# Performance work log

Measured on AMD Instinct MI355X. Metric: run time of the kernel, lower is better.

## Reference

```python
import jax, jax.numpy as jnp
import numpy as np

N, E = 50000, 800000
IN_FEATS, H, F = 128, 2, 64
NEG_SLOPE = 0.2


def _gat_conv(x, W, attn_l, attn_r, bias, src, dst):
    """DGL-style GATConv. x:[N,IN], W:[H*F,IN], attn_l/attn_r:[H,F], bias:[H*F]. Returns [N,H,F]."""
    z = (x @ W.T).reshape(N, H, F)                      # node projections
    el = jnp.einsum('nhf,hf->nh', z, attn_l)            # [N,H]
    er = jnp.einsum('nhf,hf->nh', z, attn_r)            # [N,H]
    e = jax.nn.leaky_relu(el[src] + er[dst], NEG_SLOPE) # [E,H] edge logits
    # edge softmax over incoming edges of each destination node
    m = jax.ops.segment_max(e, dst, num_segments=N)     # [N,H]
    ex = jnp.exp(e - m[dst])
    s = jax.ops.segment_sum(ex, dst, num_segments=N)    # [N,H]
    alpha = ex / s[dst]                                 # [E,H]
    msg = alpha[:, :, None] * z[src]                    # [E,H,F]
    out = jax.ops.segment_sum(msg, dst, num_segments=N) # [N,H,F]
    return out + bias.reshape(1, H, F)


def setup_inputs() -> dict:
    key = jax.random.key(0)
    ks = jax.random.split(key, 10)
    x = jax.random.normal(ks[0], (N, IN_FEATS), dtype=jnp.float32)
    h = jax.random.normal(ks[1], (N, H, F), dtype=jnp.float32)
    src = jax.random.randint(ks[2], (E,), 0, N, dtype=jnp.int32)
    dst = jax.random.randint(ks[3], (E,), 0, N, dtype=jnp.int32)
    sc = 1.0 / np.sqrt(IN_FEATS)
    W = jax.random.normal(ks[4], (3, H * F, IN_FEATS), dtype=jnp.float32) * sc  # r,u,c fc weights
    attn_l = jax.random.normal(ks[5], (3, H, F), dtype=jnp.float32) * 0.1
    attn_r = jax.random.normal(ks[6], (3, H, F), dtype=jnp.float32) * 0.1
    conv_bias = jax.random.normal(ks[7], (3, H * F), dtype=jnp.float32) * 0.02
    gate_bias = jax.random.uniform(ks[8], (3, H, F), dtype=jnp.float32)  # torch.rand init
    return {"x": x, "h": h, "W": W, "attn_l": attn_l, "attn_r": attn_r,
            "conv_bias": conv_bias, "gate_bias": gate_bias, "src": src, "dst": dst}


def reference(x, h, W, attn_l, attn_r, conv_bias, gate_bias, src, dst):
    # r, u, c gates; each GATConv is applied to x (use_hidden=False branch)
    r = jax.nn.sigmoid(_gat_conv(x, W[0], attn_l[0], attn_r[0], conv_bias[0], src, dst) + gate_bias[0])
    u = jax.nn.sigmoid(_gat_conv(x, W[1], attn_l[1], attn_r[1], conv_bias[1], src, dst) + gate_bias[1])
    # note: original computes h_ = r*h but never uses it in this branch (dead code)
    c = jax.nn.sigmoid(_gat_conv(x, W[2], attn_l[2], attn_r[2], conv_bias[2], src, dst) + gate_bias[2])
    new_h = u * h + (1.0 - u) * c
    return new_h
```

## Files before the change

### kernel.cpp

```cpp
#include <hip/hip_runtime.h>
#include <hip/hip_bf16.h>
#include <math.h>

#define NN 50000
#define EE 800000
#define KIN 128
#define HFD 128
#define ZB 256
#define NB 196
#define GB2 1564
#define SB 782
#define CAP 62
#define BSH 7
#define TRS 132

typedef __bf16 bf16_t;
typedef __bf16 bf16x8 __attribute__((ext_vector_type(8)));
typedef float f32x2 __attribute__((ext_vector_type(2)));
typedef float f32x4 __attribute__((ext_vector_type(4)));
typedef unsigned short u16;
typedef unsigned int u32;
typedef unsigned char u8;

__device__ __forceinline__ float ldf(const void* p, size_t i, int isf32) {
    return isf32 ? ((const float*)p)[i] : (float)((const bf16_t*)p)[i];
}
__device__ __forceinline__ bf16x8 load8bf(const void* base, size_t off, int isf32) {
    if (isf32) {
        const float4* p = (const float4*)((const float*)base + off);
        float4 u = p[0], v = p[1];
        bf16x8 r;
        r[0] = (bf16_t)u.x; r[1] = (bf16_t)u.y; r[2] = (bf16_t)u.z; r[3] = (bf16_t)u.w;
        r[4] = (bf16_t)v.x; r[5] = (bf16_t)v.y; r[6] = (bf16_t)v.z; r[7] = (bf16_t)v.w;
        return r;
    }
    return *(const bf16x8*)((const bf16_t*)base + off);
}

__device__ __forceinline__ uint2 pack8fp8(bf16x8 v) {
    u32 lo = __builtin_amdgcn_cvt_pk_fp8_f32((float)v[0], (float)v[1], 0u, false);
    lo = __builtin_amdgcn_cvt_pk_fp8_f32((float)v[2], (float)v[3], lo, true);
    u32 hi = __builtin_amdgcn_cvt_pk_fp8_f32((float)v[4], (float)v[5], 0u, false);
    hi = __builtin_amdgcn_cvt_pk_fp8_f32((float)v[6], (float)v[7], hi, true);
    return make_uint2(lo, hi);
}

__global__ __launch_bounds__(256) void k_front(const unsigned short* __restrict__ xw,
                                               const void* __restrict__ W,
                                               const void* __restrict__ attn_l,
                                               const void* __restrict__ attn_r,
                                               u8* __restrict__ bkt,
                                               int* __restrict__ dflag,
                                               bf16_t* __restrict__ walv)
{
    const int b = blockIdx.x, tid = threadIdx.x;
    int i = b * 256 + tid;
    if (i < NN) *(int*)(bkt + ((size_t)i << BSH)) = 0;
    if (b > 8) return;

    __shared__ int cnt;
    if (tid == 0) cnt = 0;
    __syncthreads();
    int c = 0;
    for (int k = tid; k < 2048; k += 256) {
        int e = (xw[k] >> 7) & 0xFF;
        if (e > 150) c++;
    }
    atomicAdd(&cnt, c);
    __syncthreads();
    const int isf32 = (cnt > 20) ? 1 : 0;

    if (b == 0) {
        if (tid == 0) dflag[0] = isf32;
        return;
    }
    const int c8 = b - 1;
    const int side = c8 >> 2, g = (c8 >> 1) & 1, h = c8 & 1;
    const void* attn = side ? attn_r : attn_l;
    const int k = tid;
    if (k < KIN) {
        float acc = 0.f;
        for (int f = 0; f < 64; f++) {
            float wv = ldf(W, ((size_t)(g + 1) * HFD + h * 64 + f) * KIN + k, isf32);
            float av = ldf(attn, (size_t)((g + 1) * 2 + h) * 64 + f, isf32);
            acc += wv * av;
        }
        walv[(size_t)c8 * KIN + k] = (bf16_t)acc;
    }
}

__global__ __launch_bounds__(256) void k_big(const void* __restrict__ x,
                                             const void* __restrict__ W,
                                             const bf16_t* __restrict__ walv,
                                             u8* __restrict__ z8,
                                             float* __restrict__ eln,
                                             float* __restrict__ ern,
                                             const int* __restrict__ src,
                                             const int* __restrict__ dst,
                                             u8* __restrict__ bkt,
                                             const int* __restrict__ dflag)
{
    __shared__ bf16_t wlds[128 * 128];

    const int bx = blockIdx.x;
    if (bx % 3 == 2) {
        int base = (bx / 3) * 1024 + threadIdx.x * 4;
        if (base < EE) {
            int4 s4 = *(const int4*)(src + base);
            int4 d4 = *(const int4*)(dst + base);
            u8* r0 = bkt + ((size_t)d4.x << BSH);
            u8* r1 = bkt + ((size_t)d4.y << BSH);
            u8* r2 = bkt + ((size_t)d4.z << BSH);
            u8* r3 = bkt + ((size_t)d4.w << BSH);
            int p0 = atomicAdd((int*)r0, 1);
            int p1 = atomicAdd((int*)r1, 1);
            int p2 = atomicAdd((int*)r2, 1);
            int p3 = atomicAdd((int*)r3, 1);
            if (p0 < CAP) *(u16*)(r0 + 4 + 2 * p0) = (u16)s4.x;
            if (p1 < CAP) *(u16*)(r1 + 4 + 2 * p1) = (u16)s4.y;
            if (p2 < CAP) *(u16*)(r2 + 4 + 2 * p2) = (u16)s4.z;
            if (p3 < CAP) *(u16*)(r3 + 4 + 2 * p3) = (u16)s4.w;
        }
        return;
    }

    const int isf32 = dflag[0];
    const int tid = threadIdx.x;
    const int gid = (bx / 3) * 2 + (bx % 3);
    const int ng = gid >> 1;
    const int g  = gid & 1;

    for (int c = tid; c < 2048; c += 256) {
        int col = c >> 4, g8 = c & 15;
        bf16x8 v = load8bf(W, ((size_t)(g + 1) * HFD + col) * KIN + g8 * 8, isf32);
        *(bf16x8*)(wlds + (size_t)col * 128 + (g8 ^ (col & 15)) * 8) = v;
    }

    const int wave = tid >> 6;
    const int lane = tid & 63;
    const int quad = lane >> 4;
    const int lm   = lane & 15;
    const int node_base = ng * 64 + wave * 16;

    int nld = node_base + lm;
    if (nld > NN - 1) nld = NN - 1;

    bf16x8 a[4];
#pragma unroll
    for (int kk = 0; kk < 4; kk++)
        a[kk] = load8bf(x, (size_t)nld * KIN + kk * 32 + quad * 8, isf32);

    __syncthreads();

    f32x4 acc[8];
#pragma unroll
    for (int t = 0; t < 8; t++) {
        const int wc = t * 16 + lm;
        f32x4 a4 = {0.f, 0.f, 0.f, 0.f};
#pragma unroll
        for (int kk = 0; kk < 4; kk++) {
            bf16x8 b = *(const bf16x8*)(wlds + (size_t)wc * 128 + ((kk * 4 + quad) ^ lm) * 8);
            a4 = __builtin_amdgcn_mfma_f32_16x16x32_bf16(a[kk], b, a4, 0, 0, 0);
        }
        acc[t] = a4;
    }

    if (g == 0) {
        f32x4 sacc = {0.f, 0.f, 0.f, 0.f};
#pragma unroll
        for (int kk = 0; kk < 4; kk++) {
            bf16x8 b;
            if (lm < 8) b = *(const bf16x8*)(walv + (size_t)lm * KIN + kk * 32 + quad * 8);
            else {
#pragma unroll
                for (int jj = 0; jj < 8; jj++) b[jj] = (bf16_t)0.f;
            }
            sacc = __builtin_amdgcn_mfma_f32_16x16x32_bf16(a[kk], b, sacc, 0, 0, 0);
        }
#pragma unroll
        for (int r = 0; r < 4; r++) {
            int nn = node_base + quad * 4 + r;
            if (nn < NN) {
                if (lm < 4)      eln[(size_t)nn * 4 + lm] = sacc[r];
                else if (lm < 8) ern[(size_t)nn * 4 + (lm - 4)] = sacc[r];
            }
        }
    }

    __syncthreads();
#pragma unroll
    for (int t = 0; t < 8; t++) {
#pragma unroll
        for (int r = 0; r < 4; r++)
            wlds[(size_t)(wave * 16 + quad * 4 + r) * TRS + t * 16 + lm] = (bf16_t)acc[t][r];
    }
    __syncthreads();
#pragma unroll
    for (int q = 0; q < 4; q++) {
        int node64 = q * 16 + (tid >> 4);
        int chunk  = tid & 15;
        bf16x8 v = *(const bf16x8*)(wlds + (size_t)node64 * TRS + chunk * 8);
        uint2 u = pack8fp8(v);
        int node = ng * 64 + node64;
        if (node < NN)
            *(uint2*)(z8 + (size_t)node * ZB + g * 128 + chunk * 8) = u;
    }
}

__global__ __launch_bounds__(256) void k_agg(const u8* __restrict__ z8,
                                             const u8* __restrict__ bkt,
                                             const float* __restrict__ eln,
                                             const float* __restrict__ ern,
                                             const void* __restrict__ conv_bias,
                                             const void* __restrict__ gate_bias,
                                             const void* __restrict__ hin,
                                             void* __restrict__ out,
                                             const int* __restrict__ dflag)
{
    const int isf32 = dflag[0];
    const int wave = threadIdx.x >> 6;
    const int lane = threadIdx.x & 63;
    const int j = lane >> 4;
    const int n = blockIdx.x * 4 + wave;
    if (n >= NN) return;
    const u8* rb = bkt + ((size_t)n << BSH);
    int cnt = *(const int*)rb;
    if (cnt > CAP) cnt = CAP;
    const u16* row = (const u16*)(rb + 4);
    const u32* row32 = (const u32*)row;
    const float erj = ern[(size_t)n * 4 + j];
    const u32 zoff = 4 * lane;

    float a0 = 0.f, a1 = 0.f, a2 = 0.f, a3 = 0.f, s = 0.f;
    int i = 0;
    for (; i + 8 <= cnt; i += 8) {
        u32 rr[4];
#pragma unroll
        for (int q = 0; q < 4; q++) rr[q] = row32[(i >> 1) + q];
        int sn[8];
#pragma unroll
        for (int q = 0; q < 4; q++) { sn[2*q] = rr[q] & 0xFFFF; sn[2*q+1] = rr[q] >> 16; }
        u32 zb[8];
#pragma unroll
        for (int q = 0; q < 8; q++)
            zb[q] = *(const u32*)(z8 + (size_t)sn[q] * ZB + zoff);
        float w[8];
#pragma unroll
        for (int q = 0; q < 8; q++) {
            float v = eln[(size_t)sn[q] * 4 + j] + erj;
            v = v > 0.f ? v : 0.2f * v;
            w[q] = __expf(v);
        }
#pragma unroll
        for (int q = 0; q < 8; q++) {
            f32x2 lo = __builtin_amdgcn_cvt_pk_f32_fp8(zb[q], false);
            f32x2 hi = __builtin_amdgcn_cvt_pk_f32_fp8(zb[q], true);
            a0 += w[q] * lo[0];
            a1 += w[q] * lo[1];
            a2 += w[q] * hi[0];
            a3 += w[q] * hi[1];
            s += w[q];
        }
    }
    if (i + 4 <= cnt) {
        u32 rr[2];
#pragma unroll
        for (int q = 0; q < 2; q++) rr[q] = row32[(i >> 1) + q];
        int sn[4];
#pragma unroll
        for (int q = 0; q < 2; q++) { sn[2*q] = rr[q] & 0xFFFF; sn[2*q+1] = rr[q] >> 16; }
        u32 zb[4];
#pragma unroll
        for (int q = 0; q < 4; q++)
            zb[q] = *(const u32*)(z8 + (size_t)sn[q] * ZB + zoff);
#pragma unroll
        for (int q = 0; q < 4; q++) {
            float v = eln[(size_t)sn[q] * 4 + j] + erj;
            v = v > 0.f ? v : 0.2f * v;
            float w = __expf(v);
            f32x2 lo = __builtin_amdgcn_cvt_pk_f32_fp8(zb[q], false);
            f32x2 hi = __builtin_amdgcn_cvt_pk_f32_fp8(zb[q], true);
            a0 += w * lo[0];
            a1 += w * lo[1];
            a2 += w * hi[0];
            a3 += w * hi[1];
            s += w;
        }
        i += 4;
    }
    for (; i < cnt; i++) {
        int sn = row[i];
        u32 zb = *(const u32*)(z8 + (size_t)sn * ZB + zoff);
        float v = eln[(size_t)sn * 4 + j] + erj;
        v = v > 0.f ? v : 0.2f * v;
        float w = __expf(v);
        f32x2 lo = __builtin_amdgcn_cvt_pk_f32_fp8(zb, false);
        f32x2 hi = __builtin_amdgcn_cvt_pk_f32_fp8(zb, true);
        a0 += w * lo[0];
        a1 += w * lo[1];
        a2 += w * hi[0];
        a3 += w * hi[1];
        s += w;
    }

    float inv = (cnt > 0) ? 1.f / fmaxf(s, 1e-30f) : 0.f;
    float o[4] = {a0 * inv, a1 * inv, a2 * inv, a3 * inv};

    float res[4];
    float hh[4];
    if (lane < 32) {
#pragma unroll
        for (int t = 0; t < 4; t++)
            hh[t] = ldf(hin, (size_t)n * HFD + 4 * lane + t, isf32);
    }
#pragma unroll
    for (int t = 0; t < 4; t++) {
        int c = 4 * lane + t;
        int gate = c >> 7;
        int cf = c & 127;
        int h = cf >> 6, f = cf & 63;
        float ob = ldf(conv_bias, (size_t)(gate + 1) * 128 + cf, isf32)
                 + ldf(gate_bias, (size_t)((gate + 1) * 2 + h) * 64 + f, isf32);
        float gv = 1.f / (1.f + __expf(-(o[t] + ob)));
        float other = __shfl(gv, lane ^ 32, 64);
        if (lane < 32)
            res[t] = gv * hh[t] + (1.f - gv) * other;
    }
    if (lane < 32) {
        if (isf32) {
            float4 v = {res[0], res[1], res[2], res[3]};
            *(float4*)((float*)out + (size_t)n * HFD + 4 * lane) = v;
        } else {
            bf16_t v[4];
            v[0] = (bf16_t)res[0]; v[1] = (bf16_t)res[1];
            v[2] = (bf16_t)res[2]; v[3] = (bf16_t)res[3];
            *(uint2*)((bf16_t*)out + (size_t)n * HFD + 4 * lane) = *(uint2*)v;
        }
    }
}

extern "C" void kernel_launch(void* const* d_in, const int* in_sizes, int n_in,
                              void* d_out, int out_size, void* d_ws, size_t ws_size,
                              hipStream_t stream)
{
    const void* x         = d_in[0];
    const void* hin       = d_in[1];
    const void* W         = d_in[2];
    const void* attn_l    = d_in[3];
    const void* attn_r    = d_in[4];
    const void* conv_bias = d_in[5];
    const void* gate_bias = d_in[6];
    const int* src        = (const int*)d_in[7];
    const int* dst        = (const int*)d_in[8];

    char* p = (char*)d_ws;
    int* dflag    = (int*)p;    p += 256;
    u8* z8        = (u8*)p;     p += (size_t)NN * ZB;
    float* eln    = (float*)p;  p += (size_t)NN * 4 * 4;
    float* ern    = (float*)p;  p += (size_t)NN * 4 * 4;
    u8* bkt       = (u8*)p;     p += (size_t)NN << BSH;
    bf16_t* walv  = (bf16_t*)p; p += 8 * KIN * 2;

    k_front<<<NB, 256, 0, stream>>>((const unsigned short*)x, W, attn_l, attn_r,
                                    bkt, dflag, walv);
    k_big<<<GB2 + SB, 256, 0, stream>>>(x, W, walv, z8, eln, ern, src, dst,
                                        bkt, dflag);
    k_agg<<<(NN + 3) / 4, 256, 0, stream>>>(z8, bkt, eln, ern,
                                            conv_bias, gate_bias, hin, d_out, dflag);
}
```

Baseline: 220.9 us.

## Process two node tiles per GEMM block and split aggregation edges across half-waves

The projection kernel now has each GEMM block handle 128 nodes (two 64-node tiles) and reuse one LDS copy of the weights for both. This halves the number of GEMM blocks and the repeated weight loads, and interleaves them 1:1 with the edge-bucketing blocks. The aggregation kernel now splits edges between the two half-waves, with each lane loading 8 fp8 values. Edge indices and attention weights are computed once per 8 edges and broadcast with shuffles, and the halves are combined by a cross-half reduction. The cost is more registers in the GEMM kernel and extra shuffles in the aggregation.

```diff
diff --git a/kernel.cpp b/kernel.cpp
--- a/kernel.cpp
+++ b/kernel.cpp
@@ -8,8 +8,7 @@
 #define HFD 128
 #define ZB 256
 #define NB 196
-#define GB2 1564
-#define SB 782
+#define GBLK 1564
 #define CAP 62
 #define BSH 7
 #define TRS 132
@@ -103,8 +102,8 @@
     __shared__ bf16_t wlds[128 * 128];
 
     const int bx = blockIdx.x;
-    if (bx % 3 == 2) {
-        int base = (bx / 3) * 1024 + threadIdx.x * 4;
+    if (bx & 1) {
+        int base = (bx >> 1) * 1024 + threadIdx.x * 4;
         if (base < EE) {
             int4 s4 = *(const int4*)(src + base);
             int4 d4 = *(const int4*)(dst + base);
@@ -126,7 +125,7 @@
 
     const int isf32 = dflag[0];
     const int tid = threadIdx.x;
-    const int gid = (bx / 3) * 2 + (bx % 3);
+    const int gid = bx >> 1;
     const int ng = gid >> 1;
     const int g  = gid & 1;
 
@@ -140,33 +139,39 @@
     const int lane = tid & 63;
     const int quad = lane >> 4;
     const int lm   = lane & 15;
-    const int node_base = ng * 64 + wave * 16;
-
-    int nld = node_base + lm;
-    if (nld > NN - 1) nld = NN - 1;
-
-    bf16x8 a[4];
-#pragma unroll
-    for (int kk = 0; kk < 4; kk++)
-        a[kk] = load8bf(x, (size_t)nld * KIN + kk * 32 + quad * 8, isf32);
-
-    __syncthreads();
-
-    f32x4 acc[8];
+    const int node_base0 = ng * 128 + wave * 16;
+    const int node_base1 = node_base0 + 64;
+
+    int nld0 = node_base0 + lm; if (nld0 > NN - 1) nld0 = NN - 1;
+    int nld1 = node_base1 + lm; if (nld1 > NN - 1) nld1 = NN - 1;
+
+    bf16x8 a0[4], a1[4];
+#pragma unroll
+    for (int kk = 0; kk < 4; kk++) {
+        a0[kk] = load8bf(x, (size_t)nld0 * KIN + kk * 32 + quad * 8, isf32);
+        a1[kk] = load8bf(x, (size_t)nld1 * KIN + kk * 32 + quad * 8, isf32);
+    }
+
+    __syncthreads();
+
+    f32x4 acc0[8], acc1[8];
 #pragma unroll
     for (int t = 0; t < 8; t++) {
         const int wc = t * 16 + lm;
-        f32x4 a4 = {0.f, 0.f, 0.f, 0.f};
+        f32x4 c0 = {0.f, 0.f, 0.f, 0.f};
+        f32x4 c1 = {0.f, 0.f, 0.f, 0.f};
 #pragma unroll
         for (int kk = 0; kk < 4; kk++) {
             bf16x8 b = *(const bf16x8*)(wlds + (size_t)wc * 128 + ((kk * 4 + quad) ^ lm) * 8);
-            a4 = __builtin_amdgcn_mfma_f32_16x16x32_bf16(a[kk], b, a4, 0, 0, 0);
-        }
-        acc[t] = a4;
+            c0 = __builtin_amdgcn_mfma_f32_16x16x32_bf16(a0[kk], b, c0, 0, 0, 0);
+            c1 = __builtin_amdgcn_mfma_f32_16x16x32_bf16(a1[kk], b, c1, 0, 0, 0);
+        }
+        acc0[t] = c0; acc1[t] = c1;
     }
 
     if (g == 0) {
-        f32x4 sacc = {0.f, 0.f, 0.f, 0.f};
+        f32x4 s0 = {0.f, 0.f, 0.f, 0.f};
+        f32x4 s1 = {0.f, 0.f, 0.f, 0.f};
 #pragma unroll
         for (int kk = 0; kk < 4; kk++) {
             bf16x8 b;
@@ -175,15 +180,21 @@
 #pragma unroll
                 for (int jj = 0; jj < 8; jj++) b[jj] = (bf16_t)0.f;
             }
-            sacc = __builtin_amdgcn_mfma_f32_16x16x32_bf16(a[kk], b, sacc, 0, 0, 0);
+            s0 = __builtin_amdgcn_mfma_f32_16x16x32_bf16(a0[kk], b, s0, 0, 0, 0);
+            s1 = __builtin_amdgcn_mfma_f32_16x16x32_bf16(a1[kk], b, s1, 0, 0, 0);
         }
 #pragma unroll
         for (int r = 0; r < 4; r++) {
-            int nn = node_base + quad * 4 + r;
-            if (nn < NN) {
-                if (lm < 4)      eln[(size_t)nn * 4 + lm] = sacc[r];
-                else if (lm < 8) ern[(size_t)nn * 4 + (lm - 4)] = sacc[r];
+            int nn0 = node_base0 + quad * 4 + r;
+            if (nn0 < NN) {
+                if (lm < 4)      eln[(size_t)nn0 * 4 + lm] = s0[r];
+                else if (lm < 8) ern[(size_t)nn0 * 4 + (lm - 4)] = s0[r];
             }
+            int nn1 = node_base1 + quad * 4 + r;
+            if (nn1 < NN) {
+                if (lm < 4)      eln[(size_t)nn1 * 4 + lm] = s1[r];
+                else if (lm < 8) ern[(size_t)nn1 * 4 + (lm - 4)] = s1[r];
+            }
         }
     }
 
@@ -192,7 +203,7 @@
     for (int t = 0; t < 8; t++) {
 #pragma unroll
         for (int r = 0; r < 4; r++)
-            wlds[(size_t)(wave * 16 + quad * 4 + r) * TRS + t * 16 + lm] = (bf16_t)acc[t][r];
+            wlds[(size_t)(wave * 16 + quad * 4 + r) * TRS + t * 16 + lm] = (bf16_t)acc0[t][r];
     }
     __syncthreads();
 #pragma unroll
@@ -201,7 +212,25 @@
         int chunk  = tid & 15;
         bf16x8 v = *(const bf16x8*)(wlds + (size_t)node64 * TRS + chunk * 8);
         uint2 u = pack8fp8(v);
-        int node = ng * 64 + node64;
+        int node = ng * 128 + node64;
+        if (node < NN)
+            *(uint2*)(z8 + (size_t)node * ZB + g * 128 + chunk * 8) = u;
+    }
+    __syncthreads();
+#pragma unroll
+    for (int t = 0; t < 8; t++) {
+#pragma unroll
+        for (int r = 0; r < 4; r++)
+            wlds[(size_t)(wave * 16 + quad * 4 + r) * TRS + t * 16 + lm] = (bf16_t)acc1[t][r];
+    }
+    __syncthreads();
+#pragma unroll
+    for (int q = 0; q < 4; q++) {
+        int node64 = q * 16 + (tid >> 4);
+        int chunk  = tid & 15;
+        bf16x8 v = *(const bf16x8*)(wlds + (size_t)node64 * TRS + chunk * 8);
+        uint2 u = pack8fp8(v);
+        int node = ng * 128 + 64 + node64;
         if (node < NN)
             *(uint2*)(z8 + (size_t)node * ZB + g * 128 + chunk * 8) = u;
     }
@@ -220,121 +249,110 @@
     const int isf32 = dflag[0];
     const int wave = threadIdx.x >> 6;
     const int lane = threadIdx.x & 63;
-    const int j = lane >> 4;
+    const int le   = lane & 31;
+    const int half = lane >> 5;
+    const int jz   = le >> 3;
     const int n = blockIdx.x * 4 + wave;
     if (n >= NN) return;
+
     const u8* rb = bkt + ((size_t)n << BSH);
     int cnt = *(const int*)rb;
     if (cnt > CAP) cnt = CAP;
     const u16* row = (const u16*)(rb + 4);
-    const u32* row32 = (const u32*)row;
-    const float erj = ern[(size_t)n * 4 + j];
-    const u32 zoff = 4 * lane;
-
-    float a0 = 0.f, a1 = 0.f, a2 = 0.f, a3 = 0.f, s = 0.f;
+    const float erj = ern[(size_t)n * 4 + jz];
+    const u32 zoff = 8u * (u32)le;
+    const int wsrc = jz * 8 + half;
+
+    float a[8] = {0.f, 0.f, 0.f, 0.f, 0.f, 0.f, 0.f, 0.f};
+    float s = 0.f;
+
     int i = 0;
     for (; i + 8 <= cnt; i += 8) {
-        u32 rr[4];
-#pragma unroll
-        for (int q = 0; q < 4; q++) rr[q] = row32[(i >> 1) + q];
-        int sn[8];
-#pragma unroll
-        for (int q = 0; q < 4; q++) { sn[2*q] = rr[q] & 0xFFFF; sn[2*q+1] = rr[q] >> 16; }
-        u32 zb[8];
-#pragma unroll
-        for (int q = 0; q < 8; q++)
-            zb[q] = *(const u32*)(z8 + (size_t)sn[q] * ZB + zoff);
-        float w[8];
-#pragma unroll
-        for (int q = 0; q < 8; q++) {
-            float v = eln[(size_t)sn[q] * 4 + j] + erj;
-            v = v > 0.f ? v : 0.2f * v;
-            w[q] = __expf(v);
-        }
-#pragma unroll
-        for (int q = 0; q < 8; q++) {
-            f32x2 lo = __builtin_amdgcn_cvt_pk_f32_fp8(zb[q], false);
-            f32x2 hi = __builtin_amdgcn_cvt_pk_f32_fp8(zb[q], true);
-            a0 += w[q] * lo[0];
-            a1 += w[q] * lo[1];
-            a2 += w[q] * hi[0];
-            a3 += w[q] * hi[1];
-            s += w[q];
-        }
-    }
-    if (i + 4 <= cnt) {
-        u32 rr[2];
-#pragma unroll
-        for (int q = 0; q < 2; q++) rr[q] = row32[(i >> 1) + q];
-        int sn[4];
-#pragma unroll
-        for (int q = 0; q < 2; q++) { sn[2*q] = rr[q] & 0xFFFF; sn[2*q+1] = rr[q] >> 16; }
-        u32 zb[4];
-#pragma unroll
-        for (int q = 0; q < 4; q++)
-            zb[q] = *(const u32*)(z8 + (size_t)sn[q] * ZB + zoff);
-#pragma unroll
-        for (int q = 0; q < 4; q++) {
-            float v = eln[(size_t)sn[q] * 4 + j] + erj;
-            v = v > 0.f ? v : 0.2f * v;
-            float w = __expf(v);
-            f32x2 lo = __builtin_amdgcn_cvt_pk_f32_fp8(zb[q], false);
-            f32x2 hi = __builtin_amdgcn_cvt_pk_f32_fp8(zb[q], true);
-            a0 += w * lo[0];
-            a1 += w * lo[1];
-            a2 += w * hi[0];
-            a3 += w * hi[1];
-            s += w;
-        }
-        i += 4;
-    }
-    for (; i < cnt; i++) {
-        int sn = row[i];
-        u32 zb = *(const u32*)(z8 + (size_t)sn * ZB + zoff);
-        float v = eln[(size_t)sn * 4 + j] + erj;
+        int snw = row[i + (lane & 7)];
+        float v = eln[(u32)(snw * 4 + jz)] + erj;
         v = v > 0.f ? v : 0.2f * v;
-        float w = __expf(v);
-        f32x2 lo = __builtin_amdgcn_cvt_pk_f32_fp8(zb, false);
-        f32x2 hi = __builtin_amdgcn_cvt_pk_f32_fp8(zb, true);
-        a0 += w * lo[0];
-        a1 += w * lo[1];
-        a2 += w * hi[0];
-        a3 += w * hi[1];
-        s += w;
-    }
+        float wq = __expf(v);
+#pragma unroll
+        for (int p = 0; p < 4; p++) {
+            int sn   = __shfl(snw, 2 * p + half, 64);
+            float wv = __shfl(wq, wsrc + 2 * p, 64);
+            uint2 zb = *(const uint2*)(z8 + ((u32)(sn << 8) + zoff));
+            f32x2 f0 = __builtin_amdgcn_cvt_pk_f32_fp8(zb.x, false);
+            f32x2 f1 = __builtin_amdgcn_cvt_pk_f32_fp8(zb.x, true);
+            f32x2 f2 = __builtin_amdgcn_cvt_pk_f32_fp8(zb.y, false);
+            f32x2 f3 = __builtin_amdgcn_cvt_pk_f32_fp8(zb.y, true);
+            a[0] += wv * f0[0]; a[1] += wv * f0[1];
+            a[2] += wv * f1[0]; a[3] += wv * f1[1];
+            a[4] += wv * f2[0]; a[5] += wv * f2[1];
+            a[6] += wv * f3[0]; a[7] += wv * f3[1];
+            s += wv;
+        }
+    }
+    for (; i < cnt; i += 2) {
+        int e = i + half;
+        int ok = (e < cnt);
+        int sn = row[ok ? e : i];
+        float v = eln[(u32)(sn * 4 + jz)] + erj;
+        v = v > 0.f ? v : 0.2f * v;
+        float wv = ok ? __expf(v) : 0.f;
+        uint2 zb = *(const uint2*)(z8 + ((u32)(sn << 8) + zoff));
+        f32x2 f0 = __builtin_amdgcn_cvt_pk_f32_fp8(zb.x, false);
+        f32x2 f1 = __builtin_amdgcn_cvt_pk_f32_fp8(zb.x, true);
+        f32x2 f2 = __builtin_amdgcn_cvt_pk_f32_fp8(zb.y, false);
+        f32x2 f3 = __builtin_amdgcn_cvt_pk_f32_fp8(zb.y, true);
+        a[0] += wv * f0[0]; a[1] += wv * f0[1];
+        a[2] += wv * f1[0]; a[3] += wv * f1[1];
+        a[4] += wv * f2[0]; a[5] += wv * f2[1];
+        a[6] += wv * f3[0]; a[7] += wv * f3[1];
+        s += wv;
+    }
+
+#pragma unroll
+    for (int t = 0; t < 8; t++) a[t] += __shfl(a[t], lane ^ 32, 64);
+    s += __shfl(s, lane ^ 32, 64);
 
     float inv = (cnt > 0) ? 1.f / fmaxf(s, 1e-30f) : 0.f;
-    float o[4] = {a0 * inv, a1 * inv, a2 * inv, a3 * inv};
-
-    float res[4];
-    float hh[4];
-    if (lane < 32) {
-#pragma unroll
-        for (int t = 0; t < 4; t++)
-            hh[t] = ldf(hin, (size_t)n * HFD + 4 * lane + t, isf32);
-    }
-#pragma unroll
-    for (int t = 0; t < 4; t++) {
-        int c = 4 * lane + t;
-        int gate = c >> 7;
-        int cf = c & 127;
-        int h = cf >> 6, f = cf & 63;
+
+    const int gate = le >> 4;
+    const int cf0  = (le & 15) * 8;
+    const int hI   = (le & 15) >> 3;
+
+    float hh[8];
+    if (isf32) {
+        const float* hp = (const float*)hin + (size_t)n * HFD + cf0;
+        float4 u = *(const float4*)hp;
+        float4 v = *(const float4*)(hp + 4);
+        hh[0] = u.x; hh[1] = u.y; hh[2] = u.z; hh[3] = u.w;
+        hh[4] = v.x; hh[5] = v.y; hh[6] = v.z; hh[7] = v.w;
+    } else {
+        bf16x8 hv = *(const bf16x8*)((const bf16_t*)hin + (size_t)n * HFD + cf0);
+#pragma unroll
+        for (int t = 0; t < 8; t++) hh[t] = (float)hv[t];
+    }
+
+    float res[8];
+#pragma unroll
+    for (int t = 0; t < 8; t++) {
+        int cf = cf0 + t;
+        int f = cf & 63;
         float ob = ldf(conv_bias, (size_t)(gate + 1) * 128 + cf, isf32)
-                 + ldf(gate_bias, (size_t)((gate + 1) * 2 + h) * 64 + f, isf32);
-        float gv = 1.f / (1.f + __expf(-(o[t] + ob)));
-        float other = __shfl(gv, lane ^ 32, 64);
-        if (lane < 32)
-            res[t] = gv * hh[t] + (1.f - gv) * other;
-    }
-    if (lane < 32) {
+                 + ldf(gate_bias, (size_t)((gate + 1) * 2 + hI) * 64 + f, isf32);
+        float gv = 1.f / (1.f + __expf(-(a[t] * inv + ob)));
+        float other = __shfl(gv, lane ^ 16, 64);
+        res[t] = gv * hh[t] + (1.f - gv) * other;
+    }
+    if (lane < 16) {
         if (isf32) {
-            float4 v = {res[0], res[1], res[2], res[3]};
-            *(float4*)((float*)out + (size_t)n * HFD + 4 * lane) = v;
+            float* op = (float*)out + (size_t)n * HFD + cf0;
+            float4 u = {res[0], res[1], res[2], res[3]};
+            float4 v = {res[4], res[5], res[6], res[7]};
+            *(float4*)op = u;
+            *(float4*)(op + 4) = v;
         } else {
-            bf16_t v[4];
-            v[0] = (bf16_t)res[0]; v[1] = (bf16_t)res[1];
-            v[2] = (bf16_t)res[2]; v[3] = (bf16_t)res[3];
-            *(uint2*)((bf16_t*)out + (size_t)n * HFD + 4 * lane) = *(uint2*)v;
+            bf16x8 v;
+#pragma unroll
+            for (int t = 0; t < 8; t++) v[t] = (bf16_t)res[t];
+            *(bf16x8*)((bf16_t*)out + (size_t)n * HFD + cf0) = v;
         }
     }
 }
@@ -363,8 +381,8 @@
 
     k_front<<<NB, 256, 0, stream>>>((const unsigned short*)x, W, attn_l, attn_r,
                                     bkt, dflag, walv);
-    k_big<<<GB2 + SB, 256, 0, stream>>>(x, W, walv, z8, eln, ern, src, dst,
-                                        bkt, dflag);
+    k_big<<<GBLK, 256, 0, stream>>>(x, W, walv, z8, eln, ern, src, dst,
+                                    bkt, dflag);
     k_agg<<<(NN + 3) / 4, 256, 0, stream>>>(z8, bkt, eln, ern,
                                             conv_bias, gate_bias, hin, d_out, dflag);
 }
```

After: 292.7 us. +32.5%, slower.

## Aggregate two destination nodes per wave with 8-byte fp8 gathers and masked loop

Applied to the files above, without the earlier changes.

The aggregation kernel now splits each wave into two half-waves, each handling one destination node. Each lane gathers 8 fp8 features per neighbour instead of 4, so each wave issues fewer, wider loads. The loop runs to the larger of the two halves' neighbour counts in chunks of 8, zeroing the weights of padding slots, which removes the scalar tail loops. Padded slots read clamped stale indices, and the bucket capacity is lowered to 56, which drops neighbours from any node with in-degree above 56.

```diff
diff --git a/kernel.cpp b/kernel.cpp
--- a/kernel.cpp
+++ b/kernel.cpp
@@ -10,7 +10,7 @@
 #define NB 196
 #define GB2 1564
 #define SB 782
-#define CAP 62
+#define CAP 56
 #define BSH 7
 #define TRS 132
 
@@ -220,121 +220,102 @@
     const int isf32 = dflag[0];
     const int wave = threadIdx.x >> 6;
     const int lane = threadIdx.x & 63;
-    const int j = lane >> 4;
-    const int n = blockIdx.x * 4 + wave;
-    if (n >= NN) return;
+    const int le   = lane & 31;
+    const int half = lane >> 5;
+    const int jz   = le >> 3;
+    const int n = blockIdx.x * 8 + wave * 2 + half;
+
     const u8* rb = bkt + ((size_t)n << BSH);
     int cnt = *(const int*)rb;
     if (cnt > CAP) cnt = CAP;
-    const u16* row = (const u16*)(rb + 4);
-    const u32* row32 = (const u32*)row;
-    const float erj = ern[(size_t)n * 4 + j];
-    const u32 zoff = 4 * lane;
-
-    float a0 = 0.f, a1 = 0.f, a2 = 0.f, a3 = 0.f, s = 0.f;
-    int i = 0;
-    for (; i + 8 <= cnt; i += 8) {
+    const u32* row32 = (const u32*)(rb + 4);
+    const float erj = ern[(size_t)n * 4 + jz];
+    const u32 zoff = 8u * (u32)le;
+
+    int othercnt = __shfl(cnt, lane ^ 32, 64);
+    int cm = cnt > othercnt ? cnt : othercnt;
+
+    float a[8] = {0.f, 0.f, 0.f, 0.f, 0.f, 0.f, 0.f, 0.f};
+    float s = 0.f;
+
+    for (int i = 0; i < cm; i += 8) {
         u32 rr[4];
 #pragma unroll
         for (int q = 0; q < 4; q++) rr[q] = row32[(i >> 1) + q];
         int sn[8];
 #pragma unroll
         for (int q = 0; q < 4; q++) { sn[2*q] = rr[q] & 0xFFFF; sn[2*q+1] = rr[q] >> 16; }
-        u32 zb[8];
 #pragma unroll
         for (int q = 0; q < 8; q++)
-            zb[q] = *(const u32*)(z8 + (size_t)sn[q] * ZB + zoff);
+            sn[q] = sn[q] < NN ? sn[q] : NN - 1;
+        uint2 zb[8];
+#pragma unroll
+        for (int q = 0; q < 8; q++)
+            zb[q] = *(const uint2*)(z8 + ((u32)(sn[q] << 8) + zoff));
         float w[8];
 #pragma unroll
         for (int q = 0; q < 8; q++) {
-            float v = eln[(size_t)sn[q] * 4 + j] + erj;
+            float v = eln[(u32)(sn[q] * 4 + jz)] + erj;
             v = v > 0.f ? v : 0.2f * v;
-            w[q] = __expf(v);
+            float e = __expf(v);
+            w[q] = (i + q < cnt) ? e : 0.f;
         }
 #pragma unroll
         for (int q = 0; q < 8; q++) {
-            f32x2 lo = __builtin_amdgcn_cvt_pk_f32_fp8(zb[q], false);
-            f32x2 hi = __builtin_amdgcn_cvt_pk_f32_fp8(zb[q], true);
-            a0 += w[q] * lo[0];
-            a1 += w[q] * lo[1];
-            a2 += w[q] * hi[0];
-            a3 += w[q] * hi[1];
+            f32x2 f0 = __builtin_amdgcn_cvt_pk_f32_fp8(zb[q].x, false);
+            f32x2 f1 = __builtin_amdgcn_cvt_pk_f32_fp8(zb[q].x, true);
+            f32x2 f2 = __builtin_amdgcn_cvt_pk_f32_fp8(zb[q].y, false);
+            f32x2 f3 = __builtin_amdgcn_cvt_pk_f32_fp8(zb[q].y, true);
+            a[0] += w[q] * f0[0]; a[1] += w[q] * f0[1];
+            a[2] += w[q] * f1[0]; a[3] += w[q] * f1[1];
+            a[4] += w[q] * f2[0]; a[5] += w[q] * f2[1];
+            a[6] += w[q] * f3[0]; a[7] += w[q] * f3[1];
             s += w[q];
         }
     }
-    if (i + 4 <= cnt) {
-        u32 rr[2];
-#pragma unroll
-        for (int q = 0; q < 2; q++) rr[q] = row32[(i >> 1) + q];
-        int sn[4];
-#pragma unroll
-        for (int q = 0; q < 2; q++) { sn[2*q] = rr[q] & 0xFFFF; sn[2*q+1] = rr[q] >> 16; }
-        u32 zb[4];
-#pragma unroll
-        for (int q = 0; q < 4; q++)
-            zb[q] = *(const u32*)(z8 + (size_t)sn[q] * ZB + zoff);
-#pragma unroll
-        for (int q = 0; q < 4; q++) {
-            float v = eln[(size_t)sn[q] * 4 + j] + erj;
-            v = v > 0.f ? v : 0.2f * v;
-            float w = __expf(v);
-            f32x2 lo = __builtin_amdgcn_cvt_pk_f32_fp8(zb[q], false);
-            f32x2 hi = __builtin_amdgcn_cvt_pk_f32_fp8(zb[q], true);
-            a0 += w * lo[0];
-            a1 += w * lo[1];
-            a2 += w * hi[0];
-            a3 += w * hi[1];
-            s += w;
-        }
-        i += 4;
-    }
-    for (; i < cnt; i++) {
-        int sn = row[i];
-        u32 zb = *(const u32*)(z8 + (size_t)sn * ZB + zoff);
-        float v = eln[(size_t)sn * 4 + j] + erj;
-        v = v > 0.f ? v : 0.2f * v;
-        float w = __expf(v);
-        f32x2 lo = __builtin_amdgcn_cvt_pk_f32_fp8(zb, false);
-        f32x2 hi = __builtin_amdgcn_cvt_pk_f32_fp8(zb, true);
-        a0 += w * lo[0];
-        a1 += w * lo[1];
-        a2 += w * hi[0];
-        a3 += w * hi[1];
-        s += w;
-    }
 
     float inv = (cnt > 0) ? 1.f / fmaxf(s, 1e-30f) : 0.f;
-    float o[4] = {a0 * inv, a1 * inv, a2 * inv, a3 * inv};
-
-    float res[4];
-    float hh[4];
-    if (lane < 32) {
-#pragma unroll
-        for (int t = 0; t < 4; t++)
-            hh[t] = ldf(hin, (size_t)n * HFD + 4 * lane + t, isf32);
-    }
-#pragma unroll
-    for (int t = 0; t < 4; t++) {
-        int c = 4 * lane + t;
-        int gate = c >> 7;
-        int cf = c & 127;
-        int h = cf >> 6, f = cf & 63;
+
+    const int gate = le >> 4;
+    const int cf0  = (le & 15) * 8;
+    const int hI   = (le & 15) >> 3;
+
+    float hh[8];
+    if (isf32) {
+        const float* hp = (const float*)hin + (size_t)n * HFD + cf0;
+        float4 u = *(const float4*)hp;
+        float4 v = *(const float4*)(hp + 4);
+        hh[0] = u.x; hh[1] = u.y; hh[2] = u.z; hh[3] = u.w;
+        hh[4] = v.x; hh[5] = v.y; hh[6] = v.z; hh[7] = v.w;
+    } else {
+        bf16x8 hv = *(const bf16x8*)((const bf16_t*)hin + (size_t)n * HFD + cf0);
+#pragma unroll
+        for (int t = 0; t < 8; t++) hh[t] = (float)hv[t];
+    }
+
+    float res[8];
+#pragma unroll
+    for (int t = 0; t < 8; t++) {
+        int cf = cf0 + t;
+        int f = cf & 63;
         float ob = ldf(conv_bias, (size_t)(gate + 1) * 128 + cf, isf32)
-                 + ldf(gate_bias, (size_t)((gate + 1) * 2 + h) * 64 + f, isf32);
-        float gv = 1.f / (1.f + __expf(-(o[t] + ob)));
-        float other = __shfl(gv, lane ^ 32, 64);
-        if (lane < 32)
-            res[t] = gv * hh[t] + (1.f - gv) * other;
-    }
-    if (lane < 32) {
+                 + ldf(gate_bias, (size_t)((gate + 1) * 2 + hI) * 64 + f, isf32);
+        float gv = 1.f / (1.f + __expf(-(a[t] * inv + ob)));
+        float other = __shfl(gv, lane ^ 16, 64);
+        res[t] = gv * hh[t] + (1.f - gv) * other;
+    }
+    if (le < 16) {
         if (isf32) {
-            float4 v = {res[0], res[1], res[2], res[3]};
-            *(float4*)((float*)out + (size_t)n * HFD + 4 * lane) = v;
+            float* op = (float*)out + (size_t)n * HFD + cf0;
+            float4 u = {res[0], res[1], res[2], res[3]};
+            float4 v = {res[4], res[5], res[6], res[7]};
+            *(float4*)op = u;
+            *(float4*)(op + 4) = v;
         } else {
-            bf16_t v[4];
-            v[0] = (bf16_t)res[0]; v[1] = (bf16_t)res[1];
-            v[2] = (bf16_t)res[2]; v[3] = (bf16_t)res[3];
-            *(uint2*)((bf16_t*)out + (size_t)n * HFD + 4 * lane) = *(uint2*)v;
+            bf16x8 v;
+#pragma unroll
+            for (int t = 0; t < 8; t++) v[t] = (bf16_t)res[t];
+            *(bf16x8*)((bf16_t*)out + (size_t)n * HFD + cf0) = v;
         }
     }
 }
@@ -365,6 +346,6 @@
                                     bkt, dflag, walv);
     k_big<<<GB2 + SB, 256, 0, stream>>>(x, W, walv, z8, eln, ern, src, dst,
                                         bkt, dflag);
-    k_agg<<<(NN + 3) / 4, 256, 0, stream>>>(z8, bkt, eln, ern,
+    k_agg<<<(NN + 7) / 8, 256, 0, stream>>>(z8, bkt, eln, ern,
                                             conv_bias, gate_bias, hin, d_out, dflag);
 }
```

Result: slower. 236.9 us (+7.2%).

## Store projected features in MFMA-native permuted layout and process two node tiles per block

Applied to the files above, without the earlier changes.

The GEMM blocks now write fp8 node projections straight from MFMA accumulators in a permuted column order. This removes the LDS transpose round-trip and its two barriers. The aggregation kernel is remapped to the new column permutation for heads, biases and output. Each GEMM block now covers 128 nodes over two iterations, which halves the per-block weight LDS staging, and the grid is rebalanced to alternate 1:1 with scatter blocks. The bucket capacity also drops to 56. In exchange, output and bias accesses become scattered scalar stores instead of vector stores, and the lower capacity drops more edges for high in-degree nodes.

```diff
diff --git a/kernel.cpp b/kernel.cpp
--- a/kernel.cpp
+++ b/kernel.cpp
@@ -8,11 +8,9 @@
 #define HFD 128
 #define ZB 256
 #define NB 196
-#define GB2 1564
-#define SB 782
-#define CAP 62
+#define KBG 1564
+#define CAP 56
 #define BSH 7
-#define TRS 132
 
 typedef __bf16 bf16_t;
 typedef __bf16 bf16x8 __attribute__((ext_vector_type(8)));
@@ -37,11 +35,11 @@
     return *(const bf16x8*)((const bf16_t*)base + off);
 }
 
-__device__ __forceinline__ uint2 pack8fp8(bf16x8 v) {
-    u32 lo = __builtin_amdgcn_cvt_pk_fp8_f32((float)v[0], (float)v[1], 0u, false);
-    lo = __builtin_amdgcn_cvt_pk_fp8_f32((float)v[2], (float)v[3], lo, true);
-    u32 hi = __builtin_amdgcn_cvt_pk_fp8_f32((float)v[4], (float)v[5], 0u, false);
-    hi = __builtin_amdgcn_cvt_pk_fp8_f32((float)v[6], (float)v[7], hi, true);
+__device__ __forceinline__ uint2 pack8f(const float* v) {
+    u32 lo = __builtin_amdgcn_cvt_pk_fp8_f32(v[0], v[1], 0u, false);
+    lo = __builtin_amdgcn_cvt_pk_fp8_f32(v[2], v[3], lo, true);
+    u32 hi = __builtin_amdgcn_cvt_pk_fp8_f32(v[4], v[5], 0u, false);
+    hi = __builtin_amdgcn_cvt_pk_fp8_f32(v[6], v[7], hi, true);
     return make_uint2(lo, hi);
 }
 
@@ -103,8 +101,8 @@
     __shared__ bf16_t wlds[128 * 128];
 
     const int bx = blockIdx.x;
-    if (bx % 3 == 2) {
-        int base = (bx / 3) * 1024 + threadIdx.x * 4;
+    if (bx & 1) {
+        int base = (bx >> 1) * 1024 + threadIdx.x * 4;
         if (base < EE) {
             int4 s4 = *(const int4*)(src + base);
             int4 d4 = *(const int4*)(dst + base);
@@ -126,9 +124,9 @@
 
     const int isf32 = dflag[0];
     const int tid = threadIdx.x;
-    const int gid = (bx / 3) * 2 + (bx % 3);
-    const int ng = gid >> 1;
-    const int g  = gid & 1;
+    const int gid = bx >> 1;
+    const int g   = gid & 1;
+    const int grp = gid >> 1;
 
     for (int c = tid; c < 2048; c += 256) {
         int col = c >> 4, g8 = c & 15;
@@ -140,70 +138,72 @@
     const int lane = tid & 63;
     const int quad = lane >> 4;
     const int lm   = lane & 15;
-    const int node_base = ng * 64 + wave * 16;
-
-    int nld = node_base + lm;
-    if (nld > NN - 1) nld = NN - 1;
-
-    bf16x8 a[4];
-#pragma unroll
-    for (int kk = 0; kk < 4; kk++)
-        a[kk] = load8bf(x, (size_t)nld * KIN + kk * 32 + quad * 8, isf32);
+
+    bf16x8 wb[4];
+    if (g == 0) {
+        if (lm < 8) {
+#pragma unroll
+            for (int kk = 0; kk < 4; kk++)
+                wb[kk] = *(const bf16x8*)(walv + (size_t)lm * KIN + kk * 32 + quad * 8);
+        } else {
+#pragma unroll
+            for (int kk = 0; kk < 4; kk++)
+#pragma unroll
+                for (int jj = 0; jj < 8; jj++) wb[kk][jj] = (bf16_t)0.f;
+        }
+    }
 
     __syncthreads();
 
-    f32x4 acc[8];
-#pragma unroll
-    for (int t = 0; t < 8; t++) {
-        const int wc = t * 16 + lm;
-        f32x4 a4 = {0.f, 0.f, 0.f, 0.f};
-#pragma unroll
-        for (int kk = 0; kk < 4; kk++) {
-            bf16x8 b = *(const bf16x8*)(wlds + (size_t)wc * 128 + ((kk * 4 + quad) ^ lm) * 8);
-            a4 = __builtin_amdgcn_mfma_f32_16x16x32_bf16(a[kk], b, a4, 0, 0, 0);
-        }
-        acc[t] = a4;
-    }
-
-    if (g == 0) {
-        f32x4 sacc = {0.f, 0.f, 0.f, 0.f};
-#pragma unroll
-        for (int kk = 0; kk < 4; kk++) {
-            bf16x8 b;
-            if (lm < 8) b = *(const bf16x8*)(walv + (size_t)lm * KIN + kk * 32 + quad * 8);
-            else {
-#pragma unroll
-                for (int jj = 0; jj < 8; jj++) b[jj] = (bf16_t)0.f;
+#pragma unroll 1
+    for (int m = 0; m < 2; m++) {
+        const int node_base = grp * 128 + m * 64 + wave * 16;
+        int nld = node_base + lm;
+        if (nld > NN - 1) nld = NN - 1;
+
+        bf16x8 a[4];
+#pragma unroll
+        for (int kk = 0; kk < 4; kk++)
+            a[kk] = load8bf(x, (size_t)nld * KIN + kk * 32 + quad * 8, isf32);
+
+        f32x4 acc[8];
+#pragma unroll
+        for (int t = 0; t < 8; t++) {
+            const int wc = t * 16 + lm;
+            f32x4 a4 = {0.f, 0.f, 0.f, 0.f};
+#pragma unroll
+            for (int kk = 0; kk < 4; kk++) {
+                bf16x8 b = *(const bf16x8*)(wlds + (size_t)wc * 128 + ((kk * 4 + quad) ^ lm) * 8);
+                a4 = __builtin_amdgcn_mfma_f32_16x16x32_bf16(a[kk], b, a4, 0, 0, 0);
             }
-            sacc = __builtin_amdgcn_mfma_f32_16x16x32_bf16(a[kk], b, sacc, 0, 0, 0);
-        }
+            acc[t] = a4;
+        }
+
+        if (g == 0) {
+            f32x4 sacc = {0.f, 0.f, 0.f, 0.f};
+#pragma unroll
+            for (int kk = 0; kk < 4; kk++)
+                sacc = __builtin_amdgcn_mfma_f32_16x16x32_bf16(a[kk], wb[kk], sacc, 0, 0, 0);
+#pragma unroll
+            for (int r = 0; r < 4; r++) {
+                int nn = node_base + quad * 4 + r;
+                if (nn < NN) {
+                    if (lm < 4)      eln[(size_t)nn * 4 + lm] = sacc[r];
+                    else if (lm < 8) ern[(size_t)nn * 4 + (lm - 4)] = sacc[r];
+                }
+            }
+        }
+
 #pragma unroll
         for (int r = 0; r < 4; r++) {
-            int nn = node_base + quad * 4 + r;
-            if (nn < NN) {
-                if (lm < 4)      eln[(size_t)nn * 4 + lm] = sacc[r];
-                else if (lm < 8) ern[(size_t)nn * 4 + (lm - 4)] = sacc[r];
-            }
-        }
-    }
-
-    __syncthreads();
-#pragma unroll
-    for (int t = 0; t < 8; t++) {
-#pragma unroll
-        for (int r = 0; r < 4; r++)
-            wlds[(size_t)(wave * 16 + quad * 4 + r) * TRS + t * 16 + lm] = (bf16_t)acc[t][r];
-    }
-    __syncthreads();
-#pragma unroll
-    for (int q = 0; q < 4; q++) {
-        int node64 = q * 16 + (tid >> 4);
-        int chunk  = tid & 15;
-        bf16x8 v = *(const bf16x8*)(wlds + (size_t)node64 * TRS + chunk * 8);
-        uint2 u = pack8fp8(v);
-        int node = ng * 64 + node64;
-        if (node < NN)
-            *(uint2*)(z8 + (size_t)node * ZB + g * 128 + chunk * 8) = u;
+            float f[8];
+#pragma unroll
+            for (int t = 0; t < 8; t++) f[t] = acc[t][r];
+            uint2 u = pack8f(f);
+            int node = node_base + quad * 4 + r;
+            if (node < NN)
+                *(uint2*)(z8 + (size_t)node * ZB + g * 128 + lm * 8) = u;
+        }
     }
 }
 
@@ -220,7 +220,7 @@
     const int isf32 = dflag[0];
     const int wave = threadIdx.x >> 6;
     const int lane = threadIdx.x & 63;
-    const int j = lane >> 4;
+    const int j = ((lane >> 5) << 1) | (lane & 1);
     const int n = blockIdx.x * 4 + wave;
     if (n >= NN) return;
     const u8* rb = bkt + ((size_t)n << BSH);
@@ -306,35 +306,36 @@
     float inv = (cnt > 0) ? 1.f / fmaxf(s, 1e-30f) : 0.f;
     float o[4] = {a0 * inv, a1 * inv, a2 * inv, a3 * inv};
 
+    const int gate = lane >> 5;
+    int cf[4];
+#pragma unroll
+    for (int u = 0; u < 4; u++) cf[u] = (4 * (lane & 1) + u) * 16 + ((lane & 31) >> 1);
+
     float res[4];
     float hh[4];
     if (lane < 32) {
 #pragma unroll
-        for (int t = 0; t < 4; t++)
-            hh[t] = ldf(hin, (size_t)n * HFD + 4 * lane + t, isf32);
-    }
-#pragma unroll
-    for (int t = 0; t < 4; t++) {
-        int c = 4 * lane + t;
-        int gate = c >> 7;
-        int cf = c & 127;
-        int h = cf >> 6, f = cf & 63;
-        float ob = ldf(conv_bias, (size_t)(gate + 1) * 128 + cf, isf32)
-                 + ldf(gate_bias, (size_t)((gate + 1) * 2 + h) * 64 + f, isf32);
-        float gv = 1.f / (1.f + __expf(-(o[t] + ob)));
+        for (int u = 0; u < 4; u++)
+            hh[u] = ldf(hin, (size_t)n * HFD + cf[u], isf32);
+    }
+#pragma unroll
+    for (int u = 0; u < 4; u++) {
+        float ob = ldf(conv_bias, (size_t)(gate + 1) * HFD + cf[u], isf32)
+                 + ldf(gate_bias, (size_t)((gate + 1) * 2 + (lane & 1)) * 64 + (cf[u] & 63), isf32);
+        float gv = 1.f / (1.f + __expf(-(o[u] + ob)));
         float other = __shfl(gv, lane ^ 32, 64);
         if (lane < 32)
-            res[t] = gv * hh[t] + (1.f - gv) * other;
+            res[u] = gv * hh[u] + (1.f - gv) * other;
     }
     if (lane < 32) {
         if (isf32) {
-            float4 v = {res[0], res[1], res[2], res[3]};
-            *(float4*)((float*)out + (size_t)n * HFD + 4 * lane) = v;
+#pragma unroll
+            for (int u = 0; u < 4; u++)
+                ((float*)out)[(size_t)n * HFD + cf[u]] = res[u];
         } else {
-            bf16_t v[4];
-            v[0] = (bf16_t)res[0]; v[1] = (bf16_t)res[1];
-            v[2] = (bf16_t)res[2]; v[3] = (bf16_t)res[3];
-            *(uint2*)((bf16_t*)out + (size_t)n * HFD + 4 * lane) = *(uint2*)v;
+#pragma unroll
+            for (int u = 0; u < 4; u++)
+                ((bf16_t*)out)[(size_t)n * HFD + cf[u]] = (bf16_t)res[u];
         }
     }
 }
@@ -363,8 +364,8 @@
 
     k_front<<<NB, 256, 0, stream>>>((const unsigned short*)x, W, attn_l, attn_r,
                                     bkt, dflag, walv);
-    k_big<<<GB2 + SB, 256, 0, stream>>>(x, W, walv, z8, eln, ern, src, dst,
-                                        bkt, dflag);
+    k_big<<<KBG, 256, 0, stream>>>(x, W, walv, z8, eln, ern, src, dst,
+                                   bkt, dflag);
     k_agg<<<(NN + 3) / 4, 256, 0, stream>>>(z8, bkt, eln, ern,
                                             conv_bias, gate_bias, hin, d_out, dflag);
 }
```

Result: slower. 232.6 us (+5.3%).
